# Performance work log

Measured on AMD Instinct MI355X. Metric: run time of the kernel, lower is better.

The kernel has to match this reference:

```python
import jax, jax.numpy as jnp
import numpy as np

B, C, H, W = 16, 512, 32, 32
G = 32  # GroupNorm groups
EPS = 1e-5


def setup_inputs() -> dict:
    key = jax.random.key(0)
    ks = jax.random.split(key, 10)
    s = 1.0 / np.sqrt(C)
    return {
        "x": jax.random.normal(ks[0], (B, C, H, W), dtype=jnp.float32),
        "Wq": jax.random.normal(ks[1], (C, C), dtype=jnp.float32) * s,
        "bq": jnp.zeros((C,), dtype=jnp.float32),
        "Wk": jax.random.normal(ks[2], (C, C), dtype=jnp.float32) * s,
        "bk": jnp.zeros((C,), dtype=jnp.float32),
        "Wv": jax.random.normal(ks[3], (C, C), dtype=jnp.float32) * s,
        "bv": jnp.zeros((C,), dtype=jnp.float32),
        "Wo": jax.random.normal(ks[4], (C, C), dtype=jnp.float32) * s,
        "bo": jnp.zeros((C,), dtype=jnp.float32),
        "gamma": jnp.ones((C,), dtype=jnp.float32),
        "beta": jnp.zeros((C,), dtype=jnp.float32),
    }


def _group_norm(x, gamma, beta):
    b, c, h, w = x.shape
    xg = x.reshape(b, G, c // G, h, w)
    mean = xg.mean(axis=(2, 3, 4), keepdims=True)
    var = xg.var(axis=(2, 3, 4), keepdims=True)
    xn = ((xg - mean) / jnp.sqrt(var + EPS)).reshape(b, c, h, w)
    return xn * gamma[None, :, None, None] + beta[None, :, None, None]


def _conv1x1(x, Wt, bias):
    # 1x1 conv == per-pixel GEMM over channels
    return jnp.einsum('oc,bchw->bohw', Wt, x) + bias[None, :, None, None]


def reference(x, Wq, bq, Wk, bk, Wv, bv, Wo, bo, gamma, beta):
    b, c, h, w = x.shape
    out = jax.nn.silu(_group_norm(x, gamma, beta))
    q = _conv1x1(out, Wq, bq)
    k = _conv1x1(out, Wk, bk)
    v = _conv1x1(out, Wv, bv)
    scale = float(c) ** (-0.5)
    # [b,h,w,H,W] attention scores over all spatial positions
    scores = jnp.einsum('bchw,bcHW->bhwHW', q, k) * scale
    attn = jax.nn.softmax(scores.reshape(b, h, w, h * w), axis=-1).reshape(b, h, w, h, w)
    hh = jnp.einsum('bhwHW,bcHW->bchw', attn, v)
    hh = _conv1x1(hh, Wo, bo)
    return hh + x
```

## Files before the change

kernel.cpp:

```cpp
#include <hip/hip_runtime.h>
#include <hip/hip_bf16.h>

#define HWN    1024
#define CCH    512
#define NBATCH 16
#define NGROUP 32
#define EPSV   1e-5f

using bf16 = __hip_bfloat16;
typedef __attribute__((ext_vector_type(4))) float f32x4;
typedef __attribute__((ext_vector_type(8))) short s16x8;

__device__ __forceinline__ float ldv(const void* p, long i, int c) {
    return c ? ((const float*)p)[i] : __bfloat162float(((const bf16*)p)[i]);
}
__device__ __forceinline__ void stv(void* p, long i, int c, float v) {
    if (c) ((float*)p)[i] = v;
    else   ((bf16*)p)[i]  = __float2bfloat16(v);
}
__device__ __forceinline__ float b2f(short s) {
    return __uint_as_float(((unsigned)(unsigned short)s) << 16);
}

__device__ __forceinline__ void glds16(const void* g, void* l) {
    __builtin_amdgcn_global_load_lds(
        (const __attribute__((address_space(1))) void*)g,
        (__attribute__((address_space(3))) void*)l, 16, 0, 0);
}

__global__ __launch_bounds__(256) void detect_kernel(const void* __restrict__ x,
                                                     int* __restrict__ flag)
{
    const int tid = threadIdx.x;
    const unsigned short* h = (const unsigned short*)x;
    int ok = 0;
    for (int i = tid; i < 4096; i += 256) {
        int e = (h[2 * i] >> 7) & 0xFF;
        if (e >= 100 && e <= 135) ok++;
    }
    __shared__ int red[256];
    red[tid] = ok; __syncthreads();
    for (int off = 128; off > 0; off >>= 1) {
        if (tid < off) red[tid] += red[tid + off];
        __syncthreads();
    }
    if (tid == 0) flag[0] = (red[0] < 2458) ? 1 : 0;
}

__global__ __launch_bounds__(256) void gn_stats_kernel(const void* __restrict__ x,
                                                       const int* __restrict__ flag,
                                                       float2* __restrict__ stats)
{
    const int f = flag[0];
    const int b = blockIdx.x >> 5, g = blockIdx.x & 31;
    const long base = ((long)b * CCH + (long)g * (CCH / NGROUP)) * HWN;
    const int tid = threadIdx.x;
    const int n = (CCH / NGROUP) * HWN;
    float s = 0.f, ss = 0.f;
    if (f) {
        const float4* xp = (const float4*)((const float*)x + base);
        #pragma unroll
        for (int k = 0; k < 16; ++k) {
            float4 u = xp[tid + k * 256];
            s  += u.x + u.y + u.z + u.w;
            ss += u.x * u.x + u.y * u.y + u.z * u.z + u.w * u.w;
        }
    } else {
        for (int i = tid; i < n; i += 256) {
            float v = ldv(x, base + i, 0);
            s += v; ss += v * v;
        }
    }
    __shared__ float r1[256], r2[256];
    r1[tid] = s; r2[tid] = ss; __syncthreads();
    for (int off = 128; off > 0; off >>= 1) {
        if (tid < off) { r1[tid] += r1[tid + off]; r2[tid] += r2[tid + off]; }
        __syncthreads();
    }
    if (tid == 0) {
        float mean = r1[0] / n;
        float var  = r2[0] / n - mean * mean;
        stats[blockIdx.x] = make_float2(mean, rsqrtf(var + EPSV));
    }
}

__global__ __launch_bounds__(256)
void prep_kernel(const void* __restrict__ Wq, const void* __restrict__ Wk,
                 const void* __restrict__ Wv, const void* __restrict__ Wo,
                 const void* __restrict__ bq, const void* __restrict__ bk,
                 const void* __restrict__ bv, const void* __restrict__ bo,
                 const int* __restrict__ flag,
                 bf16* __restrict__ Wqk, bf16* __restrict__ Wvb, bf16* __restrict__ Wob,
                 float* __restrict__ bQK, float* __restrict__ bV, float* __restrict__ bO)
{
    const int f = flag[0];
    const int idx = blockIdx.x * 256 + threadIdx.x;
    if (idx < 524288) {
        const int r = idx >> 9, c = idx & 511;
        float v = (r < 512) ? ldv(Wq, (long)r * 512 + c, f)
                            : ldv(Wk, (long)(r - 512) * 512 + c, f);
        Wqk[idx] = __float2bfloat16(v);
    } else if (idx < 786432) {
        Wvb[idx - 524288] = __float2bfloat16(ldv(Wv, idx - 524288, f));
    } else if (idx < 1048576) {
        Wob[idx - 786432] = __float2bfloat16(ldv(Wo, idx - 786432, f));
    } else {
        const int j = idx - 1048576;
        if      (j < 512)  bQK[j]        = ldv(bq, j, f);
        else if (j < 1024) bQK[j]        = ldv(bk, j - 512, f);
        else if (j < 1536) bV[j - 1024]  = ldv(bv, j - 1024, f);
        else if (j < 2048) bO[j - 1536]  = ldv(bo, j - 1536, f);
    }
}

__global__ __launch_bounds__(256)
void prep_t_kernel(const void* __restrict__ Wq, const void* __restrict__ Wk,
                   const void* __restrict__ Wv, const void* __restrict__ Wo,
                   const void* __restrict__ bq, const void* __restrict__ bk,
                   const void* __restrict__ bv, const void* __restrict__ bo,
                   const int* __restrict__ flag,
                   bf16* __restrict__ WkT, bf16* __restrict__ WqT,
                   bf16* __restrict__ WvT, bf16* __restrict__ Wob,
                   float* __restrict__ bqf, float* __restrict__ bkf,
                   float* __restrict__ bvf, float* __restrict__ bof)
{
    const int f = flag[0];
    const int bx = blockIdx.x;
    const int tid = threadIdx.x;
    if (bx < 192) {
        const int mat = bx >> 6;
        const void* src = mat == 0 ? Wq : mat == 1 ? Wk : Wv;
        bf16* dst = mat == 0 ? WqT : mat == 1 ? WkT : WvT;
        const int tile = bx & 63;
        const int r0 = (tile >> 3) * 64, c0 = (tile & 7) * 64;
        __shared__ float t[64][65];
        const int il = tid & 63, hq = tid >> 6;
        #pragma unroll
        for (int rr = 0; rr < 16; ++rr) {
            const int r = rr * 4 + hq;
            t[r][il] = ldv(src, (long)(r0 + r) * 512 + c0 + il, f);
        }
        __syncthreads();
        #pragma unroll
        for (int rr = 0; rr < 16; ++rr) {
            const int cc = rr * 4 + hq;
            dst[(long)(c0 + cc) * 512 + r0 + il] = __float2bfloat16(t[il][cc]);
        }
    } else if (bx < 256) {
        const int base = (bx - 192) * 4096;
        #pragma unroll
        for (int pass = 0; pass < 2; ++pass) {
            const int i = base + pass * 2048 + tid * 8;
            s16x8 out;
            if (f) {
                const float4* sp = (const float4*)Wo;
                const float4 a = sp[i >> 2];
                const float4 b = sp[(i >> 2) + 1];
                out[0] = (short)(ushort)__bfloat16_as_ushort(__float2bfloat16(a.x));
                out[1] = (short)(ushort)__bfloat16_as_ushort(__float2bfloat16(a.y));
                out[2] = (short)(ushort)__bfloat16_as_ushort(__float2bfloat16(a.z));
                out[3] = (short)(ushort)__bfloat16_as_ushort(__float2bfloat16(a.w));
                out[4] = (short)(ushort)__bfloat16_as_ushort(__float2bfloat16(b.x));
                out[5] = (short)(ushort)__bfloat16_as_ushort(__float2bfloat16(b.y));
                out[6] = (short)(ushort)__bfloat16_as_ushort(__float2bfloat16(b.z));
                out[7] = (short)(ushort)__bfloat16_as_ushort(__float2bfloat16(b.w));
            } else {
                out = *(const s16x8*)((const bf16*)Wo + i);
            }
            *(s16x8*)&Wob[i] = out;
        }
    } else {
        for (int i = tid; i < 512; i += 256) {
            bqf[i] = ldv(bq, i, f);
            bkf[i] = ldv(bk, i, f);
            bvf[i] = ldv(bv, i, f);
            bof[i] = ldv(bo, i, f);
        }
    }
}

__global__ __launch_bounds__(256)
void micro_kernel(const bf16* __restrict__ WkT, const bf16* __restrict__ WqT,
                  const bf16* __restrict__ Wob,
                  const float* __restrict__ bqf, const float* __restrict__ bkf,
                  const float* __restrict__ bvf, const float* __restrict__ bof,
                  float* __restrict__ w1, float* __restrict__ w2,
                  float* __restrict__ b2, float* __restrict__ c0)
{
    const int bx = blockIdx.x, tid = threadIdx.x;
    if (bx < 6) {
        __shared__ float vec[512];
        const float* bsrc = bx < 2 ? bqf : bx < 4 ? bkf : bvf;
        const bf16* msrc  = bx < 2 ? WkT : bx < 4 ? WqT : Wob;
        for (int i = tid; i < 512; i += 256) vec[i] = bsrc[i];
        __syncthreads();
        const int o = (bx & 1) * 256 + tid;
        const bf16* row = msrc + (long)o * 512;
        float s = 0.f;
        for (int k = 0; k < 512; k += 8) {
            s16x8 v = *(const s16x8*)&row[k];
            #pragma unroll
            for (int e = 0; e < 8; ++e) s += b2f(v[e]) * vec[k + e];
        }
        if (bx < 2)      w1[o] = s;
        else if (bx < 4) w2[o] = s;
        else             b2[o] = s + bof[o];
    } else {
        __shared__ float red[256];
        red[tid] = bqf[tid] * bkf[tid] + bqf[tid + 256] * bkf[tid + 256];
        __syncthreads();
        for (int off = 128; off > 0; off >>= 1) {
            if (tid < off) red[tid] += red[tid + off];
            __syncthreads();
        }
        if (tid == 0) c0[0] = red[0];
    }
}

__global__ __launch_bounds__(256)
void gn_apply_kernel(const void* __restrict__ x, const int* __restrict__ flag,
                     const float2* __restrict__ stats,
                     const void* __restrict__ gamma, const void* __restrict__ beta,
                     bf16* __restrict__ yx,
                     const float* __restrict__ w1, const float* __restrict__ w2,
                     float* __restrict__ rowB, float* __restrict__ colB,
                     float scale)
{
    const int f = flag[0];
    __shared__ float t[64][65];
    __shared__ float redu[4][64], redv[4][64];
    const int gx = gridDim.x, gy = gridDim.y;
    const int nwg = gx * gy * (int)gridDim.z;
    const int lin = blockIdx.x + gx * (blockIdx.y + gy * blockIdx.z);
    const int qq = nwg >> 3, rr = nwg & 7;
    const int xc = lin & 7, sq = lin >> 3;
    const int nl = (xc < rr ? xc * (qq + 1) : rr * (qq + 1) + (xc - rr) * qq) + sq;
    const int bxi = nl % gx;
    const int tt  = nl / gx;
    const int byi = tt % gy;
    const int bz  = tt / gy;

    const int i0 = bxi * 64;
    const int c0 = byi * 64;
    const int tid = threadIdx.x;
    const int il = tid & 63;
    const int hq = tid >> 6;
    float su = 0.f, sv = 0.f;
    #pragma unroll
    for (int r = 0; r < 16; ++r) {
        const int cl = r * 4 + hq;
        const int c = c0 + cl;
        const float2 st = stats[bz * NGROUP + (c >> 4)];
        const float ga = ldv(gamma, c, f), be = ldv(beta, c, f);
        float v = ldv(x, (long)bz * CCH * HWN + (long)c * HWN + i0 + il, f);
        v = (v - st.x) * st.y * ga + be;
        const float s = v / (1.f + __expf(-v));
        t[cl][il] = s;
        su += s * w1[c];
        sv += s * w2[c];
    }
    redu[hq][il] = su;
    redv[hq][il] = sv;
    __syncthreads();
    #pragma unroll
    for (int r = 0; r < 16; ++r) {
        const int ii = r * 4 + hq;
        yx[(long)bz * (HWN * (long)HWN) + (long)(i0 + ii) * 1024 + 512 + c0 + il] =
            __float2bfloat16(t[il][ii]);
    }
    if (tid < 64) {
        const float s1 = redu[0][tid] + redu[1][tid] + redu[2][tid] + redu[3][tid];
        const float s2 = redv[0][tid] + redv[1][tid] + redv[2][tid] + redv[3][tid];
        const long gi = (long)bz * HWN + i0 + tid;
        atomicAdd(&colB[gi], scale * s1);
        atomicAdd(&rowB[gi], scale * s2);
    }
}

__global__ __launch_bounds__(256)
void gn_apply_old(const void* __restrict__ x, const int* __restrict__ flag,
                  const float2* __restrict__ stats,
                  const void* __restrict__ gamma, const void* __restrict__ beta,
                  bf16* __restrict__ xn, int zb)
{
    const int f = flag[0];
    __shared__ float t[64][65];
    const int bx = zb + blockIdx.z;
    const int i0 = blockIdx.x * 64;
    const int c0 = blockIdx.y * 64;
    const int tid = threadIdx.x;
    const int il = tid & 63;
    const int hq = tid >> 6;
    #pragma unroll
    for (int r = 0; r < 16; ++r) {
        const int cl = r * 4 + hq;
        const int c = c0 + cl;
        const float2 st = stats[bx * NGROUP + (c >> 4)];
        const float ga = ldv(gamma, c, f), be = ldv(beta, c, f);
        float v = ldv(x, (long)bx * CCH * HWN + (long)c * HWN + i0 + il, f);
        v = (v - st.x) * st.y * ga + be;
        t[cl][il] = v / (1.f + __expf(-v));
    }
    __syncthreads();
    #pragma unroll
    for (int r = 0; r < 16; ++r) {
        const int ii = r * 4 + hq;
        xn[(long)blockIdx.z * CCH * HWN + (long)(i0 + ii) * CCH + c0 + il] =
            __float2bfloat16(t[il][ii]);
    }
}

template<bool FINAL, bool EXPS, bool RDIV, bool RDIVB>
__global__ __launch_bounds__(256)
void mfma_gemm(const bf16* __restrict__ A, const bf16* __restrict__ B,
               void* __restrict__ C, int K,
               int lda, int ldb, int ldc,
               long sA, long sB, long sC, int z0,
               const float* __restrict__ rowBias, long rbZ,
               const float* __restrict__ colBias, long cbZ,
               const float* __restrict__ cbase,
               float alpha, const void* __restrict__ resid, long sR,
               const int* __restrict__ flag)
{
    __shared__ bf16 lA[2][128 * 32];
    __shared__ bf16 lB[2][128 * 32];

    const int gx = gridDim.x, gy = gridDim.y;
    const int nwg = gx * gy * (int)gridDim.z;
    const int lin = blockIdx.x + gx * (blockIdx.y + gy * blockIdx.z);
    const int qq = nwg >> 3, rr = nwg & 7;
    const int xc = lin & 7, sq = lin >> 3;
    const int nl = (xc < rr ? xc * (qq + 1) : rr * (qq + 1) + (xc - rr) * qq) + sq;
    const int bxi = nl % gx;
    const int tt  = nl / gx;
    const int byi = tt % gy;
    const int bzi = tt / gy;

    const int tid = threadIdx.x;
    const int w   = tid >> 6;
    const int l   = tid & 63;
    const int ln  = l & 15;
    const int qd  = l >> 4;
    const int wm  = (w >> 1) * 64;
    const int wn  = (w & 1) * 64;
    const int zA  = z0 + bzi;

    const bf16* Ab = A + (long)zA * sA;
    const bf16* Bb = B + (long)zA * sB;
    const int m0 = byi * 128;
    const int n0 = bxi * 128;

    const int sr   = l >> 2;
    const int kswz = ((l & 3) ^ ((l >> 3) & 3)) * 8;
    const bf16* gA0 = Ab + (long)(m0 + w * 16 + sr) * lda + kswz;
    const bf16* gA1 = gA0 + (long)64 * lda;
    const bf16* gB0 = Bb + (long)(n0 + w * 16 + sr) * ldb + kswz;
    const bf16* gB1 = gB0 + (long)64 * ldb;

    f32x4 acc[4][4];
    #pragma unroll
    for (int i = 0; i < 4; ++i)
        #pragma unroll
        for (int j = 0; j < 4; ++j)
            acc[i][j] = (f32x4){0.f, 0.f, 0.f, 0.f};

    f32x4 racc[4];
    #pragma unroll
    for (int i = 0; i < 4; ++i) racc[i] = (f32x4){0.f, 0.f, 0.f, 0.f};
    s16x8 ones;
    #pragma unroll
    for (int e = 0; e < 8; ++e) ones[e] = (short)0x3F80;

    const int swA = (qd ^ ((ln >> 1) & 3)) * 8;

    glds16(gA0, &lA[0][w * 512]);
    glds16(gA1, &lA[0][2048 + w * 512]);
    glds16(gB0, &lB[0][w * 512]);
    glds16(gB1, &lB[0][2048 + w * 512]);

    const int f = (FINAL && flag) ? flag[0] : 0;
    float rs[4][4][4];
    float rbv[4][4], cbv[4];
    float cba = 0.f;
    {
        if (rowBias) {
            #pragma unroll
            for (int i = 0; i < 4; ++i)
                #pragma unroll
                for (int r = 0; r < 4; ++r)
                    rbv[i][r] = rowBias[(long)zA * rbZ + m0 + wm + i * 16 + qd * 4 + r];
        }
        if (colBias) {
            #pragma unroll
            for (int j = 0; j < 4; ++j)
                cbv[j] = colBias[(long)zA * cbZ + n0 + wn + j * 16 + ln];
            if (cbase) cba = alpha * cbase[0];
        }
        if (FINAL && resid) {
            #pragma unroll
            for (int i = 0; i < 4; ++i)
                #pragma unroll
                for (int r = 0; r < 4; ++r) {
                    const int m = m0 + wm + i * 16 + qd * 4 + r;
                    #pragma unroll
                    for (int j = 0; j < 4; ++j) {
                        const int n = n0 + wn + j * 16 + ln;
                        rs[i][r][j] = ldv(resid, (long)zA * sR + (long)m * ldc + n, f);
                    }
                }
        }
        __builtin_amdgcn_sched_barrier(0);
    }

    const int NK = K >> 5;
    for (int t = 0; t < NK; ++t) {
        const int p = t & 1;
        __syncthreads();
        if (t + 1 < NK) {
            const int kk = (t + 1) << 5;
            glds16(gA0 + kk, &lA[p ^ 1][w * 512]);
            glds16(gA1 + kk, &lA[p ^ 1][2048 + w * 512]);
            glds16(gB0 + kk, &lB[p ^ 1][w * 512]);
            glds16(gB1 + kk, &lB[p ^ 1][2048 + w * 512]);
        }
        s16x8 af[4], bfr[4];
        #pragma unroll
        for (int i = 0; i < 4; ++i)
            af[i] = *(const s16x8*)&lA[p][(wm + i * 16 + ln) * 32 + swA];
        #pragma unroll
        for (int j = 0; j < 4; ++j)
            bfr[j] = *(const s16x8*)&lB[p][(wn + j * 16 + ln) * 32 + swA];
        if (RDIV) {
            #pragma unroll
            for (int i = 0; i < 4; ++i)
                racc[i] = __builtin_amdgcn_mfma_f32_16x16x32_bf16(
                    af[i], ones, racc[i], 0, 0, 0);
        }
        if (RDIVB) {
            #pragma unroll
            for (int j = 0; j < 4; ++j)
                racc[j] = __builtin_amdgcn_mfma_f32_16x16x32_bf16(
                    ones, bfr[j], racc[j], 0, 0, 0);
        }
        #pragma unroll
        for (int i = 0; i < 4; ++i)
            #pragma unroll
            for (int j = 0; j < 4; ++j)
                acc[i][j] = __builtin_amdgcn_mfma_f32_16x16x32_bf16(
                    af[i], bfr[j], acc[i][j], 0, 0, 0);
    }

    float invb[4];
    if (RDIVB) {
        #pragma unroll
        for (int j = 0; j < 4; ++j) invb[j] = 1.f / racc[j][0];
    }

    #pragma unroll
    for (int i = 0; i < 4; ++i) {
        #pragma unroll
        for (int r = 0; r < 4; ++r) {
            const int m = m0 + wm + i * 16 + qd * 4 + r;
            const float rb = rowBias ? rbv[i][r] : 0.f;
            const float inv = RDIV ? (1.f / racc[i][r]) : 1.f;
            #pragma unroll
            for (int j = 0; j < 4; ++j) {
                const int n = n0 + wn + j * 16 + ln;
                float v = alpha * acc[i][j][r] + rb;
                if (colBias) v += cbv[j] + cba;
                if (EXPS) v = __expf(fminf(v, 60.f));
                if (RDIV) v *= inv;
                if (RDIVB) v *= invb[j];
                const long idx = (long)zA * sC + (long)m * ldc + n;
                if (FINAL) {
                    if (resid) v += rs[i][r][j];
                    stv(C, idx, f, v);
                } else {
                    ((bf16*)C)[idx] = __float2bfloat16(v);
                }
            }
        }
    }
}

extern "C" void kernel_launch(void* const* d_in, const int* in_sizes, int n_in,
                              void* d_out, int out_size, void* d_ws, size_t ws_size,
                              hipStream_t stream)
{
    const long NX = (long)NBATCH * CCH * HWN;
    int ix, iWq, ibq, iWk, ibk, iWv, ibv, iWo, ibo, iga, ibe;
    if (in_sizes[0] == NX) {
        ix = 0; iWq = 1; ibq = 2; iWk = 3; ibk = 4; iWv = 5; ibv = 6;
        iWo = 7; ibo = 8; iga = 9; ibe = 10;
    } else {
        iWk = 0; iWo = 1; iWq = 2; iWv = 3; ibe = 4; ibk = 5; ibo = 6;
        ibq = 7; ibv = 8; iga = 9; ix = 10;
    }
    const void* x     = d_in[ix];
    const void* Wq    = d_in[iWq];
    const void* bq    = d_in[ibq];
    const void* Wk    = d_in[iWk];
    const void* bk    = d_in[ibk];
    const void* Wv    = d_in[iWv];
    const void* bv    = d_in[ibv];
    const void* Wo    = d_in[iWo];
    const void* bo    = d_in[ibo];
    const void* gamma = d_in[iga];
    const void* beta  = d_in[ibe];

    const long CHW = (long)CCH * HWN;
    const long NN  = (long)HWN * HWN;
    const size_t MB = 1ull << 20;
    const size_t KB = 1024;
    char* ws = (char*)d_ws;

    dim3 blk(256);
    const float scale = 0.044194173824159216f;
    const float* FNUL = nullptr;
    const void*  VNUL = nullptr;

    if (ws_size >= 84 * MB) {
        bf16* WkT = (bf16*)ws;
        bf16* Wob = (bf16*)(ws + 512 * KB);
        bf16* WqT = (bf16*)(ws + MB);
        bf16* WvT = (bf16*)(ws + MB + 512 * KB);
        bf16* Mt  = (bf16*)(ws + 2 * MB);
        bf16* W2  = (bf16*)(ws + 2 * MB + 512 * KB);
        float*  bqf  = (float*)(ws + 3 * MB);
        float*  bkf  = (float*)(ws + 3 * MB + 2 * KB);
        float*  bvf  = (float*)(ws + 3 * MB + 4 * KB);
        float*  bof  = (float*)(ws + 3 * MB + 6 * KB);
        float*  w1   = (float*)(ws + 3 * MB + 8 * KB);
        float*  w2   = (float*)(ws + 3 * MB + 10 * KB);
        float*  b2   = (float*)(ws + 3 * MB + 12 * KB);
        float*  c0   = (float*)(ws + 3 * MB + 14 * KB);
        float2* stats= (float2*)(ws + 3 * MB + 16 * KB);
        int*    flag = (int*)(ws + 3 * MB + 20 * KB);
        float*  rowB = (float*)(ws + 3 * MB + 24 * KB);
        float*  colB = (float*)(ws + 3 * MB + 88 * KB);
        bf16* Zt = (bf16*)(ws + 4 * MB);
        bf16* S  = (bf16*)(ws + 20 * MB);
        bf16* yx = (bf16*)(ws + 52 * MB);

        detect_kernel<<<dim3(1), blk, 0, stream>>>(x, flag);
        gn_stats_kernel<<<dim3(NBATCH * NGROUP), blk, 0, stream>>>(x, flag, stats);
        prep_t_kernel<<<dim3(257), blk, 0, stream>>>(Wq, Wk, Wv, Wo, bq, bk, bv, bo,
                                                     flag, WkT, WqT, WvT, Wob,
                                                     bqf, bkf, bvf, bof);
        micro_kernel<<<dim3(7), blk, 0, stream>>>(WkT, WqT, Wob, bqf, bkf, bvf, bof,
                                                  w1, w2, b2, c0);
        mfma_gemm<false, false, false, false><<<dim3(4, 4, 2), blk, 0, stream>>>(
            WkT, WqT, Mt, 512, 512, 512, 512, 262144L, 262144L, 262144L, 0,
            FNUL, 0L, FNUL, 0L, FNUL, 1.f, VNUL, 0L, nullptr);
        hipMemsetAsync(rowB, 0, 128 * KB, stream);
        gn_apply_kernel<<<dim3(16, 8, NBATCH), blk, 0, stream>>>(
            x, flag, stats, gamma, beta, yx, w1, w2, rowB, colB, scale);
        mfma_gemm<false, false, false, false><<<dim3(8, 4, NBATCH), blk, 0, stream>>>(
            W2, yx + 512, Zt, 512, 512, 1024, 1024, 0L, NN, CHW, 0,
            b2, 0L, FNUL, 0L, FNUL, 1.f, VNUL, 0L, nullptr);
        mfma_gemm<false, false, false, false><<<dim3(4, 128, 1), blk, 0, stream>>>(
            yx + 512, Mt, yx, 512, 1024, 512, 1024, 0L, 0L, 0L, 0,
            FNUL, 0L, FNUL, 0L, FNUL, 1.f, VNUL, 0L, nullptr);
        mfma_gemm<false, true, false, false><<<dim3(8, 8, NBATCH), blk, 0, stream>>>(
            yx, yx + 512, S, 512, 1024, 1024, 1024, NN, NN, NN, 0,
            rowB, 1024L, colB, 1024L, c0, scale, VNUL, 0L, nullptr);
        mfma_gemm<true, false, false, true><<<dim3(8, 4, NBATCH), blk, 0, stream>>>(
            Zt, S, d_out, 1024, 1024, 1024, 1024, CHW, NN, CHW, 0,
            FNUL, 0L, FNUL, 0L, FNUL, 1.f, x, CHW, flag);
    } else {
        bf16*   Wqk   = (bf16*)ws;
        bf16*   Wvb   = (bf16*)(ws + MB);
        bf16*   Wob   = (bf16*)(ws + MB + MB / 2);
        float*  bQK   = (float*)(ws + 2 * MB);
        float*  bV    = (float*)(ws + 2 * MB + 4096);
        float*  bO    = (float*)(ws + 2 * MB + 6144);
        float2* stats = (float2*)(ws + 2 * MB + 8192);
        int*    flag  = (int*)(ws + 2 * MB + 12288);
        bf16* xn = (bf16*)(ws + 3 * MB);
        bf16* V  = (bf16*)(ws + 4 * MB);
        bf16* QK = (bf16*)(ws + 5 * MB);
        bf16* S  = (bf16*)(ws + 7 * MB);
        bf16* O  = xn;

        detect_kernel<<<dim3(1), blk, 0, stream>>>(x, flag);
        gn_stats_kernel<<<dim3(NBATCH * NGROUP), blk, 0, stream>>>(x, flag, stats);
        prep_kernel<<<dim3(4104), blk, 0, stream>>>(Wq, Wk, Wv, Wo, bq, bk, bv, bo,
                                                    flag, Wqk, Wvb, Wob, bQK, bV, bO);
        for (int b = 0; b < NBATCH; ++b) {
            gn_apply_old<<<dim3(16, 8, 1), blk, 0, stream>>>(
                x, flag, stats, gamma, beta, xn, b);
            mfma_gemm<false, false, false, false><<<dim3(8, 8, 1), blk, 0, stream>>>(
                xn, Wqk, QK, 512, 512, 512, 1024, 0L, 0L, 0L, 0,
                FNUL, 0L, bQK, 0L, FNUL, 1.f, VNUL, 0L, nullptr);
            mfma_gemm<false, false, false, false><<<dim3(8, 4, 1), blk, 0, stream>>>(
                Wvb, xn, V, 512, 512, 512, 1024, 0L, 0L, 0L, 0,
                bV, 0L, FNUL, 0L, FNUL, 1.f, VNUL, 0L, nullptr);
            mfma_gemm<false, true, false, false><<<dim3(8, 8, 1), blk, 0, stream>>>(
                QK, QK + 512, S, 512, 1024, 1024, 1024, 0L, 0L, 0L, b,
                FNUL, 0L, FNUL, 0L, FNUL, scale, VNUL, 0L, nullptr);
            mfma_gemm<false, false, true, false><<<dim3(4, 8, 1), blk, 0, stream>>>(
                S, V, O, 1024, 1024, 1024, 512, 0L, 0L, 0L, b,
                FNUL, 0L, FNUL, 0L, FNUL, 1.f, VNUL, 0L, nullptr);
            mfma_gemm<true, false, false, false><<<dim3(8, 4, 1), blk, 0, stream>>>(
                Wob, O, d_out, 512, 512, 512, 1024, 0L, 0L, CHW, b,
                bO, 0L, FNUL, 0L, FNUL, 1.f, x, CHW, flag);
        }
    }
}
```

Baseline: 246.5 us.

## Merge stats, weight prep and micro kernels; fuse two independent GEMMs into one launch

Combines the GroupNorm stats, weight transpose/convert, bias-vector micro precompute and the rowB/colB zeroing into one mega kernel with block-index dispatch, removing three launches and a memset. The micro precompute now reads the raw fp32 weights directly instead of the transposed bf16 copies, so it no longer depends on the prep stage. The two independent projection GEMMs (Y·Mt and W2·Y) share a single launch via a parameter-struct dual kernel, which fills the GPU better. The cost is more complex dispatch, and the micro blocks now do strided scalar loads from the fp32 weights.

```diff
diff --git a/kernel.cpp b/kernel.cpp
--- a/kernel.cpp
+++ b/kernel.cpp
@@ -47,12 +47,11 @@
     if (tid == 0) flag[0] = (red[0] < 2458) ? 1 : 0;
 }
 
-__global__ __launch_bounds__(256) void gn_stats_kernel(const void* __restrict__ x,
-                                                       const int* __restrict__ flag,
-                                                       float2* __restrict__ stats)
-{
-    const int f = flag[0];
-    const int b = blockIdx.x >> 5, g = blockIdx.x & 31;
+__device__ __forceinline__
+void gn_stats_dev(const void* __restrict__ x, int f, float2* __restrict__ stats,
+                  int bidx, float* pool)
+{
+    const int b = bidx >> 5, g = bidx & 31;
     const long base = ((long)b * CCH + (long)g * (CCH / NGROUP)) * HWN;
     const int tid = threadIdx.x;
     const int n = (CCH / NGROUP) * HWN;
@@ -71,7 +70,8 @@
             s += v; ss += v * v;
         }
     }
-    __shared__ float r1[256], r2[256];
+    float* r1 = pool;
+    float* r2 = pool + 256;
     r1[tid] = s; r2[tid] = ss; __syncthreads();
     for (int off = 128; off > 0; off >>= 1) {
         if (tid < off) { r1[tid] += r1[tid + off]; r2[tid] += r2[tid + off]; }
@@ -80,74 +80,38 @@
     if (tid == 0) {
         float mean = r1[0] / n;
         float var  = r2[0] / n - mean * mean;
-        stats[blockIdx.x] = make_float2(mean, rsqrtf(var + EPSV));
-    }
-}
-
-__global__ __launch_bounds__(256)
-void prep_kernel(const void* __restrict__ Wq, const void* __restrict__ Wk,
-                 const void* __restrict__ Wv, const void* __restrict__ Wo,
-                 const void* __restrict__ bq, const void* __restrict__ bk,
-                 const void* __restrict__ bv, const void* __restrict__ bo,
-                 const int* __restrict__ flag,
-                 bf16* __restrict__ Wqk, bf16* __restrict__ Wvb, bf16* __restrict__ Wob,
-                 float* __restrict__ bQK, float* __restrict__ bV, float* __restrict__ bO)
-{
-    const int f = flag[0];
-    const int idx = blockIdx.x * 256 + threadIdx.x;
-    if (idx < 524288) {
-        const int r = idx >> 9, c = idx & 511;
-        float v = (r < 512) ? ldv(Wq, (long)r * 512 + c, f)
-                            : ldv(Wk, (long)(r - 512) * 512 + c, f);
-        Wqk[idx] = __float2bfloat16(v);
-    } else if (idx < 786432) {
-        Wvb[idx - 524288] = __float2bfloat16(ldv(Wv, idx - 524288, f));
-    } else if (idx < 1048576) {
-        Wob[idx - 786432] = __float2bfloat16(ldv(Wo, idx - 786432, f));
-    } else {
-        const int j = idx - 1048576;
-        if      (j < 512)  bQK[j]        = ldv(bq, j, f);
-        else if (j < 1024) bQK[j]        = ldv(bk, j - 512, f);
-        else if (j < 1536) bV[j - 1024]  = ldv(bv, j - 1024, f);
-        else if (j < 2048) bO[j - 1536]  = ldv(bo, j - 1536, f);
-    }
-}
-
-__global__ __launch_bounds__(256)
-void prep_t_kernel(const void* __restrict__ Wq, const void* __restrict__ Wk,
-                   const void* __restrict__ Wv, const void* __restrict__ Wo,
-                   const void* __restrict__ bq, const void* __restrict__ bk,
-                   const void* __restrict__ bv, const void* __restrict__ bo,
-                   const int* __restrict__ flag,
-                   bf16* __restrict__ WkT, bf16* __restrict__ WqT,
-                   bf16* __restrict__ WvT, bf16* __restrict__ Wob,
-                   float* __restrict__ bqf, float* __restrict__ bkf,
-                   float* __restrict__ bvf, float* __restrict__ bof)
-{
-    const int f = flag[0];
-    const int bx = blockIdx.x;
+        stats[bidx] = make_float2(mean, rsqrtf(var + EPSV));
+    }
+}
+
+__device__ __forceinline__
+void prep_t_dev(const void* __restrict__ Wq, const void* __restrict__ Wk,
+                const void* __restrict__ Wv, const void* __restrict__ Wo,
+                int f, bf16* __restrict__ WkT, bf16* __restrict__ WqT,
+                bf16* __restrict__ WvT, bf16* __restrict__ Wob,
+                int idx, float* pool)
+{
     const int tid = threadIdx.x;
-    if (bx < 192) {
-        const int mat = bx >> 6;
+    if (idx < 192) {
+        const int mat = idx >> 6;
         const void* src = mat == 0 ? Wq : mat == 1 ? Wk : Wv;
         bf16* dst = mat == 0 ? WqT : mat == 1 ? WkT : WvT;
-        const int tile = bx & 63;
+        const int tile = idx & 63;
         const int r0 = (tile >> 3) * 64, c0 = (tile & 7) * 64;
-        __shared__ float t[64][65];
         const int il = tid & 63, hq = tid >> 6;
         #pragma unroll
         for (int rr = 0; rr < 16; ++rr) {
             const int r = rr * 4 + hq;
-            t[r][il] = ldv(src, (long)(r0 + r) * 512 + c0 + il, f);
+            pool[r * 65 + il] = ldv(src, (long)(r0 + r) * 512 + c0 + il, f);
         }
         __syncthreads();
         #pragma unroll
         for (int rr = 0; rr < 16; ++rr) {
             const int cc = rr * 4 + hq;
-            dst[(long)(c0 + cc) * 512 + r0 + il] = __float2bfloat16(t[il][cc]);
-        }
-    } else if (bx < 256) {
-        const int base = (bx - 192) * 4096;
+            dst[(long)(c0 + cc) * 512 + r0 + il] = __float2bfloat16(pool[il * 65 + cc]);
+        }
+    } else {
+        const int base = (idx - 192) * 4096;
         #pragma unroll
         for (int pass = 0; pass < 2; ++pass) {
             const int i = base + pass * 2048 + tid * 8;
@@ -169,51 +133,100 @@
             }
             *(s16x8*)&Wob[i] = out;
         }
+    }
+}
+
+__device__ __forceinline__
+void micro_raw_dev(const void* __restrict__ Wq, const void* __restrict__ Wk,
+                   const void* __restrict__ Wo,
+                   const void* __restrict__ bq, const void* __restrict__ bk,
+                   const void* __restrict__ bv, const void* __restrict__ bo,
+                   int f, float* __restrict__ w1, float* __restrict__ w2,
+                   float* __restrict__ b2, float* __restrict__ c0,
+                   float* __restrict__ rowB, float* __restrict__ colB,
+                   int idx, float* pool)
+{
+    const int tid = threadIdx.x;
+    if (idx < 6) {
+        const void* bsrc = idx < 2 ? bq : idx < 4 ? bk : bv;
+        for (int i = tid; i < 512; i += 256) pool[i] = ldv(bsrc, i, f);
+        __syncthreads();
+        const int o = (idx & 1) * 256 + tid;
+        float s = 0.f;
+        if (idx < 4) {
+            const void* M = idx < 2 ? Wk : Wq;
+            for (int k = 0; k < 512; ++k) s += ldv(M, (long)k * 512 + o, f) * pool[k];
+            if (idx < 2) w1[o] = s; else w2[o] = s;
+        } else {
+            for (int k = 0; k < 512; ++k) s += ldv(Wo, (long)o * 512 + k, f) * pool[k];
+            b2[o] = s + ldv(bo, o, f);
+        }
+    } else if (idx == 6) {
+        float p = ldv(bq, tid, f) * ldv(bk, tid, f)
+                + ldv(bq, tid + 256, f) * ldv(bk, tid + 256, f);
+        pool[tid] = p; __syncthreads();
+        for (int off = 128; off > 0; off >>= 1) {
+            if (tid < off) pool[tid] += pool[tid + off];
+            __syncthreads();
+        }
+        if (tid == 0) c0[0] = pool[0];
     } else {
-        for (int i = tid; i < 512; i += 256) {
-            bqf[i] = ldv(bq, i, f);
-            bkf[i] = ldv(bk, i, f);
-            bvf[i] = ldv(bv, i, f);
-            bof[i] = ldv(bo, i, f);
-        }
+        float4* d4 = (float4*)((idx == 7) ? rowB : colB);
+        for (int i = tid; i < 4096; i += 256) d4[i] = make_float4(0.f, 0.f, 0.f, 0.f);
     }
 }
 
 __global__ __launch_bounds__(256)
-void micro_kernel(const bf16* __restrict__ WkT, const bf16* __restrict__ WqT,
-                  const bf16* __restrict__ Wob,
-                  const float* __restrict__ bqf, const float* __restrict__ bkf,
-                  const float* __restrict__ bvf, const float* __restrict__ bof,
+void mega1_kernel(const void* __restrict__ x, const int* __restrict__ flag,
+                  float2* __restrict__ stats,
+                  const void* __restrict__ Wq, const void* __restrict__ Wk,
+                  const void* __restrict__ Wv, const void* __restrict__ Wo,
+                  const void* __restrict__ bq, const void* __restrict__ bk,
+                  const void* __restrict__ bv, const void* __restrict__ bo,
+                  bf16* __restrict__ WkT, bf16* __restrict__ WqT,
+                  bf16* __restrict__ WvT, bf16* __restrict__ Wob,
                   float* __restrict__ w1, float* __restrict__ w2,
-                  float* __restrict__ b2, float* __restrict__ c0)
-{
-    const int bx = blockIdx.x, tid = threadIdx.x;
-    if (bx < 6) {
-        __shared__ float vec[512];
-        const float* bsrc = bx < 2 ? bqf : bx < 4 ? bkf : bvf;
-        const bf16* msrc  = bx < 2 ? WkT : bx < 4 ? WqT : Wob;
-        for (int i = tid; i < 512; i += 256) vec[i] = bsrc[i];
-        __syncthreads();
-        const int o = (bx & 1) * 256 + tid;
-        const bf16* row = msrc + (long)o * 512;
-        float s = 0.f;
-        for (int k = 0; k < 512; k += 8) {
-            s16x8 v = *(const s16x8*)&row[k];
-            #pragma unroll
-            for (int e = 0; e < 8; ++e) s += b2f(v[e]) * vec[k + e];
-        }
-        if (bx < 2)      w1[o] = s;
-        else if (bx < 4) w2[o] = s;
-        else             b2[o] = s + bof[o];
+                  float* __restrict__ b2, float* __restrict__ c0,
+                  float* __restrict__ rowB, float* __restrict__ colB)
+{
+    __shared__ float pool[64 * 65];
+    const int f = flag[0];
+    const int bx = blockIdx.x;
+    if (bx < 512)
+        gn_stats_dev(x, f, stats, bx, pool);
+    else if (bx < 768)
+        prep_t_dev(Wq, Wk, Wv, Wo, f, WkT, WqT, WvT, Wob, bx - 512, pool);
+    else
+        micro_raw_dev(Wq, Wk, Wo, bq, bk, bv, bo, f, w1, w2, b2, c0,
+                      rowB, colB, bx - 768, pool);
+}
+
+__global__ __launch_bounds__(256)
+void prep_kernel(const void* __restrict__ Wq, const void* __restrict__ Wk,
+                 const void* __restrict__ Wv, const void* __restrict__ Wo,
+                 const void* __restrict__ bq, const void* __restrict__ bk,
+                 const void* __restrict__ bv, const void* __restrict__ bo,
+                 const int* __restrict__ flag,
+                 bf16* __restrict__ Wqk, bf16* __restrict__ Wvb, bf16* __restrict__ Wob,
+                 float* __restrict__ bQK, float* __restrict__ bV, float* __restrict__ bO)
+{
+    const int f = flag[0];
+    const int idx = blockIdx.x * 256 + threadIdx.x;
+    if (idx < 524288) {
+        const int r = idx >> 9, c = idx & 511;
+        float v = (r < 512) ? ldv(Wq, (long)r * 512 + c, f)
+                            : ldv(Wk, (long)(r - 512) * 512 + c, f);
+        Wqk[idx] = __float2bfloat16(v);
+    } else if (idx < 786432) {
+        Wvb[idx - 524288] = __float2bfloat16(ldv(Wv, idx - 524288, f));
+    } else if (idx < 1048576) {
+        Wob[idx - 786432] = __float2bfloat16(ldv(Wo, idx - 786432, f));
     } else {
-        __shared__ float red[256];
-        red[tid] = bqf[tid] * bkf[tid] + bqf[tid + 256] * bkf[tid + 256];
-        __syncthreads();
-        for (int off = 128; off > 0; off >>= 1) {
-            if (tid < off) red[tid] += red[tid + off];
-            __syncthreads();
-        }
-        if (tid == 0) c0[0] = red[0];
+        const int j = idx - 1048576;
+        if      (j < 512)  bQK[j]        = ldv(bq, j, f);
+        else if (j < 1024) bQK[j]        = ldv(bk, j - 512, f);
+        else if (j < 1536) bV[j - 1024]  = ldv(bv, j - 1024, f);
+        else if (j < 2048) bO[j - 1536]  = ldv(bo, j - 1536, f);
     }
 }
 
@@ -311,30 +324,20 @@
 }
 
 template<bool FINAL, bool EXPS, bool RDIV, bool RDIVB>
-__global__ __launch_bounds__(256)
-void mfma_gemm(const bf16* __restrict__ A, const bf16* __restrict__ B,
-               void* __restrict__ C, int K,
-               int lda, int ldb, int ldc,
-               long sA, long sB, long sC, int z0,
-               const float* __restrict__ rowBias, long rbZ,
-               const float* __restrict__ colBias, long cbZ,
-               const float* __restrict__ cbase,
-               float alpha, const void* __restrict__ resid, long sR,
-               const int* __restrict__ flag)
+__device__ __forceinline__
+void gemm_dev(const bf16* __restrict__ A, const bf16* __restrict__ B,
+              void* __restrict__ C, int K,
+              int lda, int ldb, int ldc,
+              long sA, long sB, long sC, int z0,
+              const float* __restrict__ rowBias, long rbZ,
+              const float* __restrict__ colBias, long cbZ,
+              const float* __restrict__ cbase,
+              float alpha, const void* __restrict__ resid, long sR,
+              const int* __restrict__ flag,
+              int bxi, int byi, int bzi)
 {
     __shared__ bf16 lA[2][128 * 32];
     __shared__ bf16 lB[2][128 * 32];
-
-    const int gx = gridDim.x, gy = gridDim.y;
-    const int nwg = gx * gy * (int)gridDim.z;
-    const int lin = blockIdx.x + gx * (blockIdx.y + gy * blockIdx.z);
-    const int qq = nwg >> 3, rr = nwg & 7;
-    const int xc = lin & 7, sq = lin >> 3;
-    const int nl = (xc < rr ? xc * (qq + 1) : rr * (qq + 1) + (xc - rr) * qq) + sq;
-    const int bxi = nl % gx;
-    const int tt  = nl / gx;
-    const int byi = tt % gy;
-    const int bzi = tt / gy;
 
     const int tid = threadIdx.x;
     const int w   = tid >> 6;
@@ -483,6 +486,61 @@
     }
 }
 
+template<bool FINAL, bool EXPS, bool RDIV, bool RDIVB>
+__global__ __launch_bounds__(256)
+void mfma_gemm(const bf16* __restrict__ A, const bf16* __restrict__ B,
+               void* __restrict__ C, int K,
+               int lda, int ldb, int ldc,
+               long sA, long sB, long sC, int z0,
+               const float* __restrict__ rowBias, long rbZ,
+               const float* __restrict__ colBias, long cbZ,
+               const float* __restrict__ cbase,
+               float alpha, const void* __restrict__ resid, long sR,
+               const int* __restrict__ flag)
+{
+    const int gx = gridDim.x, gy = gridDim.y;
+    const int nwg = gx * gy * (int)gridDim.z;
+    const int lin = blockIdx.x + gx * (blockIdx.y + gy * blockIdx.z);
+    const int qq = nwg >> 3, rr = nwg & 7;
+    const int xc = lin & 7, sq = lin >> 3;
+    const int nl = (xc < rr ? xc * (qq + 1) : rr * (qq + 1) + (xc - rr) * qq) + sq;
+    const int bxi = nl % gx;
+    const int tt  = nl / gx;
+    const int byi = tt % gy;
+    const int bzi = tt / gy;
+    gemm_dev<FINAL, EXPS, RDIV, RDIVB>(A, B, C, K, lda, ldb, ldc, sA, sB, sC, z0,
+                                       rowBias, rbZ, colBias, cbZ, cbase, alpha,
+                                       resid, sR, flag, bxi, byi, bzi);
+}
+
+struct GemmP {
+    const bf16* A; const bf16* B; void* C;
+    int K, lda, ldb, ldc;
+    long sA, sB, sC;
+    const float* rowBias; long rbZ;
+    int gx, gy, nblk;
+};
+
+__global__ __launch_bounds__(256)
+void dual_gemm_kernel(GemmP a, GemmP b)
+{
+    const int lin = blockIdx.x;
+    const GemmP& p = (lin < a.nblk) ? a : b;
+    const int sub  = (lin < a.nblk) ? lin : lin - a.nblk;
+    const int nwg = p.nblk;
+    const int qq = nwg >> 3, rr = nwg & 7;
+    const int xc = sub & 7, sq = sub >> 3;
+    const int nl = (xc < rr ? xc * (qq + 1) : rr * (qq + 1) + (xc - rr) * qq) + sq;
+    const int bxi = nl % p.gx;
+    const int tt  = nl / p.gx;
+    const int byi = tt % p.gy;
+    const int bzi = tt / p.gy;
+    gemm_dev<false, false, false, false>(p.A, p.B, p.C, p.K, p.lda, p.ldb, p.ldc,
+                                         p.sA, p.sB, p.sC, 0,
+                                         p.rowBias, p.rbZ, nullptr, 0L, nullptr,
+                                         1.f, nullptr, 0L, nullptr, bxi, byi, bzi);
+}
+
 extern "C" void kernel_launch(void* const* d_in, const int* in_sizes, int n_in,
                               void* d_out, int out_size, void* d_ws, size_t ws_size,
                               hipStream_t stream)
@@ -526,10 +584,6 @@
         bf16* WvT = (bf16*)(ws + MB + 512 * KB);
         bf16* Mt  = (bf16*)(ws + 2 * MB);
         bf16* W2  = (bf16*)(ws + 2 * MB + 512 * KB);
-        float*  bqf  = (float*)(ws + 3 * MB);
-        float*  bkf  = (float*)(ws + 3 * MB + 2 * KB);
-        float*  bvf  = (float*)(ws + 3 * MB + 4 * KB);
-        float*  bof  = (float*)(ws + 3 * MB + 6 * KB);
         float*  w1   = (float*)(ws + 3 * MB + 8 * KB);
         float*  w2   = (float*)(ws + 3 * MB + 10 * KB);
         float*  b2   = (float*)(ws + 3 * MB + 12 * KB);
@@ -543,24 +597,28 @@
         bf16* yx = (bf16*)(ws + 52 * MB);
 
         detect_kernel<<<dim3(1), blk, 0, stream>>>(x, flag);
-        gn_stats_kernel<<<dim3(NBATCH * NGROUP), blk, 0, stream>>>(x, flag, stats);
-        prep_t_kernel<<<dim3(257), blk, 0, stream>>>(Wq, Wk, Wv, Wo, bq, bk, bv, bo,
-                                                     flag, WkT, WqT, WvT, Wob,
-                                                     bqf, bkf, bvf, bof);
-        micro_kernel<<<dim3(7), blk, 0, stream>>>(WkT, WqT, Wob, bqf, bkf, bvf, bof,
-                                                  w1, w2, b2, c0);
+        mega1_kernel<<<dim3(777), blk, 0, stream>>>(
+            x, flag, stats, Wq, Wk, Wv, Wo, bq, bk, bv, bo,
+            WkT, WqT, WvT, Wob, w1, w2, b2, c0, rowB, colB);
         mfma_gemm<false, false, false, false><<<dim3(4, 4, 2), blk, 0, stream>>>(
             WkT, WqT, Mt, 512, 512, 512, 512, 262144L, 262144L, 262144L, 0,
             FNUL, 0L, FNUL, 0L, FNUL, 1.f, VNUL, 0L, nullptr);
-        hipMemsetAsync(rowB, 0, 128 * KB, stream);
         gn_apply_kernel<<<dim3(16, 8, NBATCH), blk, 0, stream>>>(
             x, flag, stats, gamma, beta, yx, w1, w2, rowB, colB, scale);
-        mfma_gemm<false, false, false, false><<<dim3(8, 4, NBATCH), blk, 0, stream>>>(
-            W2, yx + 512, Zt, 512, 512, 1024, 1024, 0L, NN, CHW, 0,
-            b2, 0L, FNUL, 0L, FNUL, 1.f, VNUL, 0L, nullptr);
-        mfma_gemm<false, false, false, false><<<dim3(4, 128, 1), blk, 0, stream>>>(
-            yx + 512, Mt, yx, 512, 1024, 512, 1024, 0L, 0L, 0L, 0,
-            FNUL, 0L, FNUL, 0L, FNUL, 1.f, VNUL, 0L, nullptr);
+        {
+            GemmP py, pz;
+            py.A = yx + 512; py.B = Mt; py.C = yx;
+            py.K = 512; py.lda = 1024; py.ldb = 512; py.ldc = 1024;
+            py.sA = 0L; py.sB = 0L; py.sC = 0L;
+            py.rowBias = nullptr; py.rbZ = 0L;
+            py.gx = 4; py.gy = 128; py.nblk = 512;
+            pz.A = W2; pz.B = yx + 512; pz.C = Zt;
+            pz.K = 512; pz.lda = 512; pz.ldb = 1024; pz.ldc = 1024;
+            pz.sA = 0L; pz.sB = NN; pz.sC = CHW;
+            pz.rowBias = b2; pz.rbZ = 0L;
+            pz.gx = 8; pz.gy = 4; pz.nblk = 512;
+            dual_gemm_kernel<<<dim3(1024), blk, 0, stream>>>(py, pz);
+        }
         mfma_gemm<false, true, false, false><<<dim3(8, 8, NBATCH), blk, 0, stream>>>(
             yx, yx + 512, S, 512, 1024, 1024, 1024, NN, NN, NN, 0,
             rowB, 1024L, colB, 1024L, c0, scale, VNUL, 0L, nullptr);
@@ -583,7 +641,10 @@
         bf16* O  = xn;
 
         detect_kernel<<<dim3(1), blk, 0, stream>>>(x, flag);
-        gn_stats_kernel<<<dim3(NBATCH * NGROUP), blk, 0, stream>>>(x, flag, stats);
+        mega1_kernel<<<dim3(512), blk, 0, stream>>>(
+            x, flag, stats, Wq, Wk, Wv, Wo, bq, bk, bv, bo,
+            nullptr, nullptr, nullptr, nullptr,
+            nullptr, nullptr, nullptr, nullptr, nullptr, nullptr);
         prep_kernel<<<dim3(4104), blk, 0, stream>>>(Wq, Wk, Wv, Wo, bq, bk, bv, bo,
                                                     flag, Wqk, Wvb, Wob, bQK, bV, bO);
         for (int b = 0; b < NBATCH; ++b) {
```

Measured after the change: 278.0 us. +12.8%, slower.
